# Kernel optimization log

Measured on AMD Instinct MI355X. Metric: run time of the kernel, lower is better.

The kernel has to match this reference:

```python
import jax, jax.numpy as jnp
import numpy as np

HEADS = 8
DIM_HEAD = 64
SCALE = DIM_HEAD ** (-0.5)


def setup_inputs() -> dict:
    key = jax.random.key(0)
    ks = jax.random.split(key, 7)
    b, n, m = 4, 2048, 1024
    qd, cd, inner = 1024, 768, HEADS * DIM_HEAD
    s = lambda fan_in: 1.0 / np.sqrt(fan_in)
    return {
        "x": jax.random.normal(ks[0], (b, n, qd), jnp.float32),
        "context": jax.random.normal(ks[1], (b, m, cd), jnp.float32),
        "Wq": jax.random.normal(ks[2], (qd, inner), jnp.float32) * s(qd),
        "Wk": jax.random.normal(ks[3], (cd, inner), jnp.float32) * s(cd),
        "Wv": jax.random.normal(ks[4], (cd, inner), jnp.float32) * s(cd),
        "Wout": jax.random.normal(ks[5], (inner, qd), jnp.float32) * s(inner),
        "bout": jax.random.normal(ks[6], (qd,), jnp.float32) * 0.01,
    }


def reference(x, context, Wq, Wk, Wv, Wout, bout):
    b, n, _ = x.shape
    m = context.shape[1]
    # projections, then split heads: [b, s, h, d]
    q = (x @ Wq).reshape(b, n, HEADS, DIM_HEAD)
    k = (context @ Wk).reshape(b, m, HEADS, DIM_HEAD)
    v = (context @ Wv).reshape(b, m, HEADS, DIM_HEAD)
    # sim: [b, h, n, m]
    sim = jnp.einsum("bihd,bjhd->bhij", q, k) * SCALE
    attn = jax.nn.softmax(sim, axis=-1)
    out = jnp.einsum("bhij,bjhd->bihd", attn, v).reshape(b, n, HEADS * DIM_HEAD)
    return out @ Wout + bout
```

## Files before the change

### kernel.cpp

```cpp
#include <hip/hip_runtime.h>


typedef __bf16 bf16x8_t __attribute__((ext_vector_type(8)));
typedef __bf16 bf16x4_t __attribute__((ext_vector_type(4)));
typedef float  f32x4_t  __attribute__((ext_vector_type(4)));

#define GLOAD_LDS16(gptr, lptr)                                                  \
  __builtin_amdgcn_global_load_lds(                                              \
      (const __attribute__((address_space(1))) void*)(gptr),                     \
      (__attribute__((address_space(3))) void*)(lptr), 16, 0, 0)

__global__ __launch_bounds__(256) void prep_cast(const float* __restrict__ x,
                                                 __bf16* __restrict__ xb,
                                                 const float* __restrict__ ctx,
                                                 __bf16* __restrict__ cb) {
  const int NX = 8192 * 1024 / 8;
  int g = blockIdx.x * 256 + threadIdx.x;
  const float* src;
  __bf16* dst;
  if (g < NX) { src = x; dst = xb; }
  else        { src = ctx; dst = cb; g -= NX; }
  size_t i = (size_t)g * 8;
  float4 a = *(const float4*)(src + i);
  float4 b = *(const float4*)(src + i + 4);
  bf16x8_t v;
  v[0] = (__bf16)a.x; v[1] = (__bf16)a.y; v[2] = (__bf16)a.z; v[3] = (__bf16)a.w;
  v[4] = (__bf16)b.x; v[5] = (__bf16)b.y; v[6] = (__bf16)b.z; v[7] = (__bf16)b.w;
  *(bf16x8_t*)(dst + i) = v;
}

__global__ __launch_bounds__(256) void prep_weights(const float* __restrict__ Wq,
                                                    const float* __restrict__ Wk,
                                                    const float* __restrict__ Wv,
                                                    const float* __restrict__ Wout,
                                                    __bf16* __restrict__ WqT,
                                                    __bf16* __restrict__ WkvT,
                                                    __bf16* __restrict__ WoutT,
                                                    float qscale) {
  __shared__ float tile[32][33];
  int bid = blockIdx.x;
  const float* src; __bf16* dst; int R, C; float scale; int t;
  if (bid < 512)       { src = Wq;   dst = WqT;   R = 1024; C = 512;  scale = qscale; t = bid; }
  else if (bid < 896)  { src = Wk;   dst = WkvT;  R = 768;  C = 512;  scale = 1.f; t = bid - 512; }
  else if (bid < 1280) { src = Wv;   dst = WkvT + (size_t)512 * 768; R = 768; C = 512; scale = 1.f; t = bid - 896; }
  else                 { src = Wout; dst = WoutT; R = 512;  C = 1024; scale = 1.f; t = bid - 1280; }
  int tilesX = C >> 5;
  int c0 = (t % tilesX) * 32, r0 = (t / tilesX) * 32;
  int tx = threadIdx.x & 31, ty = threadIdx.x >> 5;
#pragma unroll
  for (int i = 0; i < 32; i += 8)
    tile[ty + i][tx] = src[(size_t)(r0 + ty + i) * C + (c0 + tx)];
  __syncthreads();
#pragma unroll
  for (int i = 0; i < 32; i += 8)
    dst[(size_t)(c0 + ty + i) * R + (r0 + tx)] = (__bf16)(tile[tx][ty + i] * scale);
}

__global__ __launch_bounds__(256) void proj_gemm(const __bf16* __restrict__ xb,
                                                 const __bf16* __restrict__ WqT,
                                                 __bf16* __restrict__ Qs,
                                                 const __bf16* __restrict__ cb,
                                                 const __bf16* __restrict__ WkvT,
                                                 __bf16* __restrict__ Ks,
                                                 __bf16* __restrict__ Vt) {
  __shared__ __align__(16) __bf16 As[128 * 32];
  __shared__ __align__(16) __bf16 Bs[64 * 32];
  const int bid = blockIdx.x;
  const bool isQ = (bid & 1) == 0;
  const int idx = bid >> 1;
  const __bf16 *A, *B;
  __bf16* C;
  int K, bm, bn;
  if (isQ) { A = xb; B = WqT;  C = Qs; K = 1024; bm = (idx >> 3) * 128; bn = (idx & 7) * 64; }
  else     { A = cb; B = WkvT; C = Ks; K = 768;  bm = (idx >> 4) * 128; bn = (idx & 15) * 64; }

  const int tid  = threadIdx.x;
  const int wave = tid >> 6;
  const int lane = tid & 63;
  const int quad = lane >> 4;
  const int l16  = lane & 15;
  const int wm = (wave >> 1) * 64;
  const int wn = (wave & 1) * 32;
  const int sRow = tid >> 2;
  const int sCol = (tid & 3) * 8;

  f32x4_t acc[4][2] = {};

  for (int kk = 0; kk < K; kk += 32) {
    __syncthreads();
    GLOAD_LDS16(A + (size_t)(bm + sRow) * K + kk + sCol,      As + wave * 512);
    GLOAD_LDS16(A + (size_t)(bm + 64 + sRow) * K + kk + sCol, As + 2048 + wave * 512);
    GLOAD_LDS16(B + (size_t)(bn + sRow) * K + kk + sCol,      Bs + wave * 512);
    __syncthreads();
    bf16x8_t af[4], bf[2];
#pragma unroll
    for (int i = 0; i < 4; ++i)
      af[i] = *(const bf16x8_t*)(As + (wm + i * 16 + l16) * 32 + quad * 8);
#pragma unroll
    for (int j = 0; j < 2; ++j)
      bf[j] = *(const bf16x8_t*)(Bs + (wn + j * 16 + l16) * 32 + quad * 8);
#pragma unroll
    for (int i = 0; i < 4; ++i)
#pragma unroll
      for (int j = 0; j < 2; ++j)
        acc[i][j] = __builtin_amdgcn_mfma_f32_16x16x32_bf16(af[i], bf[j], acc[i][j], 0, 0, 0);
  }

#pragma unroll
  for (int i = 0; i < 4; ++i) {
    int row = bm + wm + i * 16 + quad * 4;
#pragma unroll
    for (int j = 0; j < 2; ++j) {
      int col = bn + wn + j * 16 + l16;
      f32x4_t v = acc[i][j];
      if (isQ || col < 512) {
#pragma unroll
        for (int r = 0; r < 4; ++r) C[(size_t)(row + r) * 512 + col] = (__bf16)v[r];
      } else {
        int dg = col - 512;
        int bb = row >> 10, m0 = row & 1023;
        bf16x4_t pk;
        pk[0] = (__bf16)v[0]; pk[1] = (__bf16)v[1];
        pk[2] = (__bf16)v[2]; pk[3] = (__bf16)v[3];
        *(bf16x4_t*)(Vt + ((size_t)bb * 512 + dg) * 1024 + m0) = pk;
      }
    }
  }
}

__global__ __launch_bounds__(256) void gemm_out64(const __bf16* __restrict__ A,
                                                  const __bf16* __restrict__ B,
                                                  float* __restrict__ C,
                                                  const float* __restrict__ bias) {
  __shared__ __align__(16) __bf16 As[128 * 32];
  __shared__ __align__(16) __bf16 Bs[64 * 32];
  const int K = 512, N = 1024;
  const int tid  = threadIdx.x;
  const int wave = tid >> 6;
  const int lane = tid & 63;
  const int quad = lane >> 4;
  const int l16  = lane & 15;
  const int wm = (wave >> 1) * 64;
  const int wn = (wave & 1) * 32;
  const int bm = blockIdx.x * 128;
  const int bn = blockIdx.y * 64;
  const int sRow = tid >> 2;
  const int sCol = (tid & 3) * 8;

  f32x4_t acc[4][2] = {};

  for (int kk = 0; kk < K; kk += 32) {
    __syncthreads();
    GLOAD_LDS16(A + (size_t)(bm + sRow) * K + kk + sCol,      As + wave * 512);
    GLOAD_LDS16(A + (size_t)(bm + 64 + sRow) * K + kk + sCol, As + 2048 + wave * 512);
    GLOAD_LDS16(B + (size_t)(bn + sRow) * K + kk + sCol,      Bs + wave * 512);
    __syncthreads();
    bf16x8_t af[4], bf[2];
#pragma unroll
    for (int i = 0; i < 4; ++i)
      af[i] = *(const bf16x8_t*)(As + (wm + i * 16 + l16) * 32 + quad * 8);
#pragma unroll
    for (int j = 0; j < 2; ++j)
      bf[j] = *(const bf16x8_t*)(Bs + (wn + j * 16 + l16) * 32 + quad * 8);
#pragma unroll
    for (int i = 0; i < 4; ++i)
#pragma unroll
      for (int j = 0; j < 2; ++j)
        acc[i][j] = __builtin_amdgcn_mfma_f32_16x16x32_bf16(af[i], bf[j], acc[i][j], 0, 0, 0);
  }

#pragma unroll
  for (int i = 0; i < 4; ++i) {
    int row = bm + wm + i * 16 + quad * 4;
#pragma unroll
    for (int j = 0; j < 2; ++j) {
      int col = bn + wn + j * 16 + l16;
      float bb = bias[col];
      f32x4_t v = acc[i][j];
#pragma unroll
      for (int r = 0; r < 4; ++r) C[(size_t)(row + r) * N + col] = v[r] + bb;
    }
  }
}

__global__ __launch_bounds__(256, 2) void attn_kernel(const __bf16* __restrict__ Q,
                                                      const __bf16* __restrict__ K,
                                                      const __bf16* __restrict__ Vt,
                                                      __bf16* __restrict__ O) {
  const int hb = blockIdx.x, h = hb >> 2, b = hb & 3;
  const int qt = blockIdx.y;
  const int tid = threadIdx.x, wave = tid >> 6, lane = tid & 63;
  const int quad = lane >> 4, l16 = lane & 15;

  __shared__ __align__(16) __bf16 Ps[4][32 * 72];
  __bf16* myP = Ps[wave];

  const int q0 = qt * 128 + wave * 32;

  bf16x8_t qa[2][2];
#pragma unroll
  for (int t = 0; t < 2; ++t)
#pragma unroll
    for (int hf = 0; hf < 2; ++hf)
      qa[t][hf] = *(const bf16x8_t*)(Q + (size_t)(b * 2048 + q0 + t * 16 + l16) * 512 +
                                     h * 64 + hf * 32 + quad * 8);

  const __bf16* Kb = K + (size_t)b * 1024 * 512 + h * 64;
  const __bf16* Vb = Vt + (size_t)b * 512 * 1024 + (size_t)h * 64 * 1024;

  f32x4_t oacc[2][4] = {};
  float lpart[2][4] = {};

  bf16x8_t kf[2][4][2];
#pragma unroll
  for (int nt = 0; nt < 4; ++nt)
#pragma unroll
    for (int hf = 0; hf < 2; ++hf)
      kf[0][nt][hf] = *(const bf16x8_t*)(Kb + (size_t)(nt * 16 + l16) * 512 +
                                         hf * 32 + quad * 8);

#pragma unroll 2
  for (int it = 0; it < 16; ++it) {
    const int cur = it & 1, nxt = cur ^ 1;
    const int mm = it * 64;

    f32x4_t s[2][4];
#pragma unroll
    for (int t = 0; t < 2; ++t)
#pragma unroll
      for (int nt = 0; nt < 4; ++nt) {
        f32x4_t z = {};
        z = __builtin_amdgcn_mfma_f32_16x16x32_bf16(qa[t][0], kf[cur][nt][0], z, 0, 0, 0);
        s[t][nt] = __builtin_amdgcn_mfma_f32_16x16x32_bf16(qa[t][1], kf[cur][nt][1], z, 0, 0, 0);
      }

    bf16x8_t vf[4][2];
#pragma unroll
    for (int dt = 0; dt < 4; ++dt)
#pragma unroll
      for (int hf = 0; hf < 2; ++hf)
        vf[dt][hf] = *(const bf16x8_t*)(Vb + (size_t)(dt * 16 + l16) * 1024 +
                                        mm + hf * 32 + quad * 8);

    if (it < 15) {
#pragma unroll
      for (int nt = 0; nt < 4; ++nt)
#pragma unroll
        for (int hf = 0; hf < 2; ++hf)
          kf[nxt][nt][hf] = *(const bf16x8_t*)(Kb + (size_t)(mm + 64 + nt * 16 + l16) * 512 +
                                               hf * 32 + quad * 8);
    }

#pragma unroll
    for (int t = 0; t < 2; ++t)
#pragma unroll
      for (int nt = 0; nt < 4; ++nt)
#pragma unroll
        for (int r = 0; r < 4; ++r) {
          float pf = __builtin_exp2f(s[t][nt][r]);
          lpart[t][r] += pf;
          myP[(t * 16 + quad * 4 + r) * 72 + nt * 16 + l16] = (__bf16)pf;
        }

    bf16x8_t pa[2][2];
#pragma unroll
    for (int t = 0; t < 2; ++t)
#pragma unroll
      for (int hf = 0; hf < 2; ++hf)
        pa[t][hf] = *(const bf16x8_t*)(myP + (t * 16 + l16) * 72 + hf * 32 + quad * 8);

#pragma unroll
    for (int t = 0; t < 2; ++t)
#pragma unroll
      for (int dt = 0; dt < 4; ++dt) {
        oacc[t][dt] = __builtin_amdgcn_mfma_f32_16x16x32_bf16(pa[t][0], vf[dt][0], oacc[t][dt], 0, 0, 0);
        oacc[t][dt] = __builtin_amdgcn_mfma_f32_16x16x32_bf16(pa[t][1], vf[dt][1], oacc[t][dt], 0, 0, 0);
      }
  }

#pragma unroll
  for (int t = 0; t < 2; ++t)
#pragma unroll
    for (int r = 0; r < 4; ++r) {
      float v = lpart[t][r];
      v += __shfl_xor(v, 1, 64);
      v += __shfl_xor(v, 2, 64);
      v += __shfl_xor(v, 4, 64);
      v += __shfl_xor(v, 8, 64);
      float inv = 1.f / v;
      size_t orow = (size_t)(b * 2048 + q0 + t * 16 + quad * 4 + r) * 512 + h * 64;
#pragma unroll
      for (int dt = 0; dt < 4; ++dt)
        O[orow + dt * 16 + l16] = (__bf16)(oacc[t][dt][r] * inv);
    }
}

extern "C" void kernel_launch(void* const* d_in, const int* in_sizes, int n_in,
                              void* d_out, int out_size, void* d_ws, size_t ws_size,
                              hipStream_t stream) {
  const float* x    = (const float*)d_in[0];
  const float* ctx  = (const float*)d_in[1];
  const float* Wq   = (const float*)d_in[2];
  const float* Wk   = (const float*)d_in[3];
  const float* Wv   = (const float*)d_in[4];
  const float* Wout = (const float*)d_in[5];
  const float* bout = (const float*)d_in[6];
  float* out = (float*)d_out;

  char* ws = (char*)d_ws;
  size_t off = 0;
  auto alloc = [&](size_t bytes) {
    void* p = ws + off;
    off = (off + bytes + 255) & ~(size_t)255;
    return p;
  };
  __bf16* xb    = (__bf16*)alloc((size_t)8192 * 1024 * 2);
  __bf16* cb    = (__bf16*)alloc((size_t)4096 * 768 * 2);
  __bf16* WqT   = (__bf16*)alloc((size_t)512 * 1024 * 2);
  __bf16* WkvT  = (__bf16*)alloc((size_t)1024 * 768 * 2);
  __bf16* WoutT = (__bf16*)alloc((size_t)1024 * 512 * 2);
  __bf16* Qs    = (__bf16*)alloc((size_t)8192 * 512 * 2);
  __bf16* Ks    = (__bf16*)alloc((size_t)4096 * 512 * 2);
  __bf16* Vt    = (__bf16*)alloc((size_t)4 * 512 * 1024 * 2);
  __bf16* Os    = (__bf16*)alloc((size_t)8192 * 512 * 2);

  const float QSCALE = 0.125f * 1.4426950408889634f;

  prep_cast<<<5632, 256, 0, stream>>>(x, xb, ctx, cb);
  prep_weights<<<1792, 256, 0, stream>>>(Wq, Wk, Wv, Wout, WqT, WkvT, WoutT, QSCALE);
  proj_gemm<<<1024, 256, 0, stream>>>(xb, WqT, Qs, cb, WkvT, Ks, Vt);
  attn_kernel<<<dim3(32, 16), 256, 0, stream>>>(Qs, Ks, Vt, Os);
  gemm_out64<<<dim3(64, 16), 256, 0, stream>>>(Os, WoutT, out, bout);
}
```

Before: 210.7 us.

## Enlarge GEMM tiles to 128x128 and shrink attention work per wave

Both projection and output GEMMs move from 128x64 to 128x128 block tiles, so each wave holds a 4x4 MFMA accumulator grid and the grid is halved. This raises arithmetic intensity per LDS load. The attention kernel now gives each wave 16 query rows instead of 32, doubles the grid, and raises the occupancy hint to 4. It drops the K register double-buffering and computes the softmax row sums with an MFMA against a ones vector instead of shuffles. Risks are higher register pressure in the GEMMs and weaker latency hiding in attention now that K prefetch is gone.

```diff
diff --git a/kernel.cpp b/kernel.cpp
--- a/kernel.cpp
+++ b/kernel.cpp
@@ -64,15 +64,14 @@
                                                  __bf16* __restrict__ Ks,
                                                  __bf16* __restrict__ Vt) {
   __shared__ __align__(16) __bf16 As[128 * 32];
-  __shared__ __align__(16) __bf16 Bs[64 * 32];
+  __shared__ __align__(16) __bf16 Bs[128 * 32];
   const int bid = blockIdx.x;
-  const bool isQ = (bid & 1) == 0;
-  const int idx = bid >> 1;
+  const bool isQ = bid < 256;
+  const int idx = isQ ? bid : bid - 256;
   const __bf16 *A, *B;
-  __bf16* C;
   int K, bm, bn;
-  if (isQ) { A = xb; B = WqT;  C = Qs; K = 1024; bm = (idx >> 3) * 128; bn = (idx & 7) * 64; }
-  else     { A = cb; B = WkvT; C = Ks; K = 768;  bm = (idx >> 4) * 128; bn = (idx & 15) * 64; }
+  if (isQ) { A = xb; B = WqT;  K = 1024; bm = (idx >> 2) * 128; bn = (idx & 3) * 128; }
+  else     { A = cb; B = WkvT; K = 768;  bm = (idx >> 3) * 128; bn = (idx & 7) * 128; }
 
   const int tid  = threadIdx.x;
   const int wave = tid >> 6;
@@ -80,29 +79,30 @@
   const int quad = lane >> 4;
   const int l16  = lane & 15;
   const int wm = (wave >> 1) * 64;
-  const int wn = (wave & 1) * 32;
+  const int wn = (wave & 1) * 64;
   const int sRow = tid >> 2;
   const int sCol = (tid & 3) * 8;
 
-  f32x4_t acc[4][2] = {};
+  f32x4_t acc[4][4] = {};
 
   for (int kk = 0; kk < K; kk += 32) {
     __syncthreads();
-    GLOAD_LDS16(A + (size_t)(bm + sRow) * K + kk + sCol,      As + wave * 512);
-    GLOAD_LDS16(A + (size_t)(bm + 64 + sRow) * K + kk + sCol, As + 2048 + wave * 512);
-    GLOAD_LDS16(B + (size_t)(bn + sRow) * K + kk + sCol,      Bs + wave * 512);
+#pragma unroll
+    for (int it = 0; it < 2; ++it) {
+      GLOAD_LDS16(A + (size_t)(bm + it * 64 + sRow) * K + kk + sCol, As + it * 2048 + wave * 512);
+      GLOAD_LDS16(B + (size_t)(bn + it * 64 + sRow) * K + kk + sCol, Bs + it * 2048 + wave * 512);
+    }
     __syncthreads();
-    bf16x8_t af[4], bf[2];
+    bf16x8_t af[4], bf[4];
+#pragma unroll
+    for (int i = 0; i < 4; ++i) {
+      af[i] = *(const bf16x8_t*)(As + (wm + i * 16 + l16) * 32 + quad * 8);
+      bf[i] = *(const bf16x8_t*)(Bs + (wn + i * 16 + l16) * 32 + quad * 8);
+    }
 #pragma unroll
     for (int i = 0; i < 4; ++i)
-      af[i] = *(const bf16x8_t*)(As + (wm + i * 16 + l16) * 32 + quad * 8);
-#pragma unroll
-    for (int j = 0; j < 2; ++j)
-      bf[j] = *(const bf16x8_t*)(Bs + (wn + j * 16 + l16) * 32 + quad * 8);
-#pragma unroll
-    for (int i = 0; i < 4; ++i)
-#pragma unroll
-      for (int j = 0; j < 2; ++j)
+#pragma unroll
+      for (int j = 0; j < 4; ++j)
         acc[i][j] = __builtin_amdgcn_mfma_f32_16x16x32_bf16(af[i], bf[j], acc[i][j], 0, 0, 0);
   }
 
@@ -110,12 +110,15 @@
   for (int i = 0; i < 4; ++i) {
     int row = bm + wm + i * 16 + quad * 4;
 #pragma unroll
-    for (int j = 0; j < 2; ++j) {
+    for (int j = 0; j < 4; ++j) {
       int col = bn + wn + j * 16 + l16;
       f32x4_t v = acc[i][j];
-      if (isQ || col < 512) {
-#pragma unroll
-        for (int r = 0; r < 4; ++r) C[(size_t)(row + r) * 512 + col] = (__bf16)v[r];
+      if (isQ) {
+#pragma unroll
+        for (int r = 0; r < 4; ++r) Qs[(size_t)(row + r) * 512 + col] = (__bf16)v[r];
+      } else if (col < 512) {
+#pragma unroll
+        for (int r = 0; r < 4; ++r) Ks[(size_t)(row + r) * 512 + col] = (__bf16)v[r];
       } else {
         int dg = col - 512;
         int bb = row >> 10, m0 = row & 1023;
@@ -128,12 +131,12 @@
   }
 }
 
-__global__ __launch_bounds__(256) void gemm_out64(const __bf16* __restrict__ A,
-                                                  const __bf16* __restrict__ B,
-                                                  float* __restrict__ C,
-                                                  const float* __restrict__ bias) {
+__global__ __launch_bounds__(256) void gemm_out(const __bf16* __restrict__ A,
+                                                const __bf16* __restrict__ B,
+                                                float* __restrict__ C,
+                                                const float* __restrict__ bias) {
   __shared__ __align__(16) __bf16 As[128 * 32];
-  __shared__ __align__(16) __bf16 Bs[64 * 32];
+  __shared__ __align__(16) __bf16 Bs[128 * 32];
   const int K = 512, N = 1024;
   const int tid  = threadIdx.x;
   const int wave = tid >> 6;
@@ -141,31 +144,32 @@
   const int quad = lane >> 4;
   const int l16  = lane & 15;
   const int wm = (wave >> 1) * 64;
-  const int wn = (wave & 1) * 32;
+  const int wn = (wave & 1) * 64;
   const int bm = blockIdx.x * 128;
-  const int bn = blockIdx.y * 64;
+  const int bn = blockIdx.y * 128;
   const int sRow = tid >> 2;
   const int sCol = (tid & 3) * 8;
 
-  f32x4_t acc[4][2] = {};
+  f32x4_t acc[4][4] = {};
 
   for (int kk = 0; kk < K; kk += 32) {
     __syncthreads();
-    GLOAD_LDS16(A + (size_t)(bm + sRow) * K + kk + sCol,      As + wave * 512);
-    GLOAD_LDS16(A + (size_t)(bm + 64 + sRow) * K + kk + sCol, As + 2048 + wave * 512);
-    GLOAD_LDS16(B + (size_t)(bn + sRow) * K + kk + sCol,      Bs + wave * 512);
+#pragma unroll
+    for (int it = 0; it < 2; ++it) {
+      GLOAD_LDS16(A + (size_t)(bm + it * 64 + sRow) * K + kk + sCol, As + it * 2048 + wave * 512);
+      GLOAD_LDS16(B + (size_t)(bn + it * 64 + sRow) * K + kk + sCol, Bs + it * 2048 + wave * 512);
+    }
     __syncthreads();
-    bf16x8_t af[4], bf[2];
+    bf16x8_t af[4], bf[4];
+#pragma unroll
+    for (int i = 0; i < 4; ++i) {
+      af[i] = *(const bf16x8_t*)(As + (wm + i * 16 + l16) * 32 + quad * 8);
+      bf[i] = *(const bf16x8_t*)(Bs + (wn + i * 16 + l16) * 32 + quad * 8);
+    }
 #pragma unroll
     for (int i = 0; i < 4; ++i)
-      af[i] = *(const bf16x8_t*)(As + (wm + i * 16 + l16) * 32 + quad * 8);
-#pragma unroll
-    for (int j = 0; j < 2; ++j)
-      bf[j] = *(const bf16x8_t*)(Bs + (wn + j * 16 + l16) * 32 + quad * 8);
-#pragma unroll
-    for (int i = 0; i < 4; ++i)
-#pragma unroll
-      for (int j = 0; j < 2; ++j)
+#pragma unroll
+      for (int j = 0; j < 4; ++j)
         acc[i][j] = __builtin_amdgcn_mfma_f32_16x16x32_bf16(af[i], bf[j], acc[i][j], 0, 0, 0);
   }
 
@@ -173,7 +177,7 @@
   for (int i = 0; i < 4; ++i) {
     int row = bm + wm + i * 16 + quad * 4;
 #pragma unroll
-    for (int j = 0; j < 2; ++j) {
+    for (int j = 0; j < 4; ++j) {
       int col = bn + wn + j * 16 + l16;
       float bb = bias[col];
       f32x4_t v = acc[i][j];
@@ -183,7 +187,7 @@
   }
 }
 
-__global__ __launch_bounds__(256, 2) void attn_kernel(const __bf16* __restrict__ Q,
+__global__ __launch_bounds__(256, 4) void attn_kernel(const __bf16* __restrict__ Q,
                                                       const __bf16* __restrict__ K,
                                                       const __bf16* __restrict__ Vt,
                                                       __bf16* __restrict__ O) {
@@ -192,47 +196,43 @@
   const int tid = threadIdx.x, wave = tid >> 6, lane = tid & 63;
   const int quad = lane >> 4, l16 = lane & 15;
 
-  __shared__ __align__(16) __bf16 Ps[4][32 * 72];
+  __shared__ __align__(16) __bf16 Ps[4][16 * 72];
   __bf16* myP = Ps[wave];
 
-  const int q0 = qt * 128 + wave * 32;
-
-  bf16x8_t qa[2][2];
-#pragma unroll
-  for (int t = 0; t < 2; ++t)
-#pragma unroll
-    for (int hf = 0; hf < 2; ++hf)
-      qa[t][hf] = *(const bf16x8_t*)(Q + (size_t)(b * 2048 + q0 + t * 16 + l16) * 512 +
-                                     h * 64 + hf * 32 + quad * 8);
+  const int q0 = qt * 64 + wave * 16;
+
+  bf16x8_t qa[2];
+#pragma unroll
+  for (int hf = 0; hf < 2; ++hf)
+    qa[hf] = *(const bf16x8_t*)(Q + (size_t)(b * 2048 + q0 + l16) * 512 +
+                                h * 64 + hf * 32 + quad * 8);
 
   const __bf16* Kb = K + (size_t)b * 1024 * 512 + h * 64;
   const __bf16* Vb = Vt + (size_t)b * 512 * 1024 + (size_t)h * 64 * 1024;
 
-  f32x4_t oacc[2][4] = {};
-  float lpart[2][4] = {};
-
-  bf16x8_t kf[2][4][2];
-#pragma unroll
-  for (int nt = 0; nt < 4; ++nt)
-#pragma unroll
-    for (int hf = 0; hf < 2; ++hf)
-      kf[0][nt][hf] = *(const bf16x8_t*)(Kb + (size_t)(nt * 16 + l16) * 512 +
-                                         hf * 32 + quad * 8);
-
-#pragma unroll 2
-  for (int it = 0; it < 16; ++it) {
-    const int cur = it & 1, nxt = cur ^ 1;
-    const int mm = it * 64;
-
-    f32x4_t s[2][4];
-#pragma unroll
-    for (int t = 0; t < 2; ++t)
-#pragma unroll
-      for (int nt = 0; nt < 4; ++nt) {
-        f32x4_t z = {};
-        z = __builtin_amdgcn_mfma_f32_16x16x32_bf16(qa[t][0], kf[cur][nt][0], z, 0, 0, 0);
-        s[t][nt] = __builtin_amdgcn_mfma_f32_16x16x32_bf16(qa[t][1], kf[cur][nt][1], z, 0, 0, 0);
-      }
+  bf16x8_t ones;
+#pragma unroll
+  for (int j = 0; j < 8; ++j) ones[j] = (__bf16)1.0f;
+
+  f32x4_t oacc[4] = {};
+  f32x4_t lacc = {};
+
+  for (int mm = 0; mm < 1024; mm += 64) {
+    bf16x8_t kf[4][2];
+#pragma unroll
+    for (int nt = 0; nt < 4; ++nt)
+#pragma unroll
+      for (int hf = 0; hf < 2; ++hf)
+        kf[nt][hf] = *(const bf16x8_t*)(Kb + (size_t)(mm + nt * 16 + l16) * 512 +
+                                        hf * 32 + quad * 8);
+
+    f32x4_t s[4];
+#pragma unroll
+    for (int nt = 0; nt < 4; ++nt) {
+      f32x4_t z = {};
+      z = __builtin_amdgcn_mfma_f32_16x16x32_bf16(qa[0], kf[nt][0], z, 0, 0, 0);
+      s[nt] = __builtin_amdgcn_mfma_f32_16x16x32_bf16(qa[1], kf[nt][1], z, 0, 0, 0);
+    }
 
     bf16x8_t vf[4][2];
 #pragma unroll
@@ -242,57 +242,35 @@
         vf[dt][hf] = *(const bf16x8_t*)(Vb + (size_t)(dt * 16 + l16) * 1024 +
                                         mm + hf * 32 + quad * 8);
 
-    if (it < 15) {
-#pragma unroll
-      for (int nt = 0; nt < 4; ++nt)
-#pragma unroll
-        for (int hf = 0; hf < 2; ++hf)
-          kf[nxt][nt][hf] = *(const bf16x8_t*)(Kb + (size_t)(mm + 64 + nt * 16 + l16) * 512 +
-                                               hf * 32 + quad * 8);
-    }
-
-#pragma unroll
-    for (int t = 0; t < 2; ++t)
-#pragma unroll
-      for (int nt = 0; nt < 4; ++nt)
-#pragma unroll
-        for (int r = 0; r < 4; ++r) {
-          float pf = __builtin_exp2f(s[t][nt][r]);
-          lpart[t][r] += pf;
-          myP[(t * 16 + quad * 4 + r) * 72 + nt * 16 + l16] = (__bf16)pf;
-        }
-
-    bf16x8_t pa[2][2];
-#pragma unroll
-    for (int t = 0; t < 2; ++t)
-#pragma unroll
-      for (int hf = 0; hf < 2; ++hf)
-        pa[t][hf] = *(const bf16x8_t*)(myP + (t * 16 + l16) * 72 + hf * 32 + quad * 8);
-
-#pragma unroll
-    for (int t = 0; t < 2; ++t)
-#pragma unroll
-      for (int dt = 0; dt < 4; ++dt) {
-        oacc[t][dt] = __builtin_amdgcn_mfma_f32_16x16x32_bf16(pa[t][0], vf[dt][0], oacc[t][dt], 0, 0, 0);
-        oacc[t][dt] = __builtin_amdgcn_mfma_f32_16x16x32_bf16(pa[t][1], vf[dt][1], oacc[t][dt], 0, 0, 0);
-      }
-  }
-
-#pragma unroll
-  for (int t = 0; t < 2; ++t)
-#pragma unroll
-    for (int r = 0; r < 4; ++r) {
-      float v = lpart[t][r];
-      v += __shfl_xor(v, 1, 64);
-      v += __shfl_xor(v, 2, 64);
-      v += __shfl_xor(v, 4, 64);
-      v += __shfl_xor(v, 8, 64);
-      float inv = 1.f / v;
-      size_t orow = (size_t)(b * 2048 + q0 + t * 16 + quad * 4 + r) * 512 + h * 64;
-#pragma unroll
-      for (int dt = 0; dt < 4; ++dt)
-        O[orow + dt * 16 + l16] = (__bf16)(oacc[t][dt][r] * inv);
-    }
+#pragma unroll
+    for (int nt = 0; nt < 4; ++nt)
+#pragma unroll
+      for (int r = 0; r < 4; ++r)
+        myP[(quad * 4 + r) * 72 + nt * 16 + l16] = (__bf16)__builtin_exp2f(s[nt][r]);
+
+    bf16x8_t pa[2];
+#pragma unroll
+    for (int hf = 0; hf < 2; ++hf)
+      pa[hf] = *(const bf16x8_t*)(myP + l16 * 72 + hf * 32 + quad * 8);
+
+    lacc = __builtin_amdgcn_mfma_f32_16x16x32_bf16(pa[0], ones, lacc, 0, 0, 0);
+    lacc = __builtin_amdgcn_mfma_f32_16x16x32_bf16(pa[1], ones, lacc, 0, 0, 0);
+
+#pragma unroll
+    for (int dt = 0; dt < 4; ++dt) {
+      oacc[dt] = __builtin_amdgcn_mfma_f32_16x16x32_bf16(pa[0], vf[dt][0], oacc[dt], 0, 0, 0);
+      oacc[dt] = __builtin_amdgcn_mfma_f32_16x16x32_bf16(pa[1], vf[dt][1], oacc[dt], 0, 0, 0);
+    }
+  }
+
+#pragma unroll
+  for (int r = 0; r < 4; ++r) {
+    float inv = 1.f / lacc[r];
+    size_t orow = (size_t)(b * 2048 + q0 + quad * 4 + r) * 512 + h * 64;
+#pragma unroll
+    for (int dt = 0; dt < 4; ++dt)
+      O[orow + dt * 16 + l16] = (__bf16)(oacc[dt][r] * inv);
+  }
 }
 
 extern "C" void kernel_launch(void* const* d_in, const int* in_sizes, int n_in,
@@ -328,7 +306,7 @@
 
   prep_cast<<<5632, 256, 0, stream>>>(x, xb, ctx, cb);
   prep_weights<<<1792, 256, 0, stream>>>(Wq, Wk, Wv, Wout, WqT, WkvT, WoutT, QSCALE);
-  proj_gemm<<<1024, 256, 0, stream>>>(xb, WqT, Qs, cb, WkvT, Ks, Vt);
-  attn_kernel<<<dim3(32, 16), 256, 0, stream>>>(Qs, Ks, Vt, Os);
-  gemm_out64<<<dim3(64, 16), 256, 0, stream>>>(Os, WoutT, out, bout);
-}
+  proj_gemm<<<512, 256, 0, stream>>>(xb, WqT, Qs, cb, WkvT, Ks, Vt);
+  attn_kernel<<<dim3(32, 32), 256, 0, stream>>>(Qs, Ks, Vt, Os);
+  gemm_out<<<dim3(64, 8), 256, 0, stream>>>(Os, WoutT, out, bout);
+}
```

Measured after the change: 267.9 us. 27.1% more time.
